# Kernel optimization log

Hardware: AMD Instinct MI355X
Metric: run time of the kernel (lower is better)

Reference implementation:

```python
import jax, jax.numpy as jnp
import numpy as np

B, N = 128, 64
HID, MLP, DS, DV = 128, 128, 32, 32
DH = MLP - DS - DV  # 64
FILL = -10.0


def _embed_mask(x, W, b, fill):
    # Linear+ReLU on non-NaN rows; fill NaN rows with `fill` (matches embed_with_masking).
    nan = jnp.isnan(x).any(-1)
    e = jax.nn.relu(jnp.where(jnp.isnan(x), 0.0, x) @ W + b)
    return jnp.where(nan[..., None], jnp.asarray(fill, x.dtype), e)


def setup_inputs() -> dict:
    key = jax.random.key(0)
    ks = jax.random.split(key, 12)
    s = 0.05
    return {
        "hidden_states": jax.random.normal(ks[0], (B, N, HID), jnp.float32),
        "obs1": jax.random.normal(ks[1], (B, N, 2), jnp.float32),
        "obs2": jax.random.normal(ks[2], (B, N, 2), jnp.float32),
        "w_sp": jax.random.normal(ks[3], (2, DS), jnp.float32) * s,
        "b_sp": jnp.zeros((DS,), jnp.float32),
        "w_vel": jax.random.normal(ks[4], (2, DV), jnp.float32) * s,
        "b_vel": jnp.zeros((DV,), jnp.float32),
        "w_hid": jax.random.normal(ks[5], (HID, DH), jnp.float32) * s,
        "b_hid": jnp.zeros((DH,), jnp.float32),
        "wq": jax.random.normal(ks[6], (MLP, MLP), jnp.float32) * s,
        "wk": jax.random.normal(ks[7], (MLP, MLP), jnp.float32) * s,
        "wv": jax.random.normal(ks[8], (MLP, MLP), jnp.float32) * s,
        "in_proj_w": jax.random.normal(ks[9], (MLP, 3 * MLP), jnp.float32) * s,
        "in_proj_b": jnp.zeros((3 * MLP,), jnp.float32),
        "mha_out_w": jax.random.normal(ks[10], (MLP, MLP), jnp.float32) * s,
        "mha_out_b": jnp.zeros((MLP,), jnp.float32),
        "out_w": jax.random.normal(ks[11], (MLP, MLP), jnp.float32) * s,
        "out_b": jnp.zeros((MLP,), jnp.float32),
    }


def reference(hidden_states, obs1, obs2, w_sp, b_sp, w_vel, b_vel, w_hid, b_hid,
              wq, wk, wv, in_proj_w, in_proj_b, mha_out_w, mha_out_b, out_w, out_b):
    b, n = obs2.shape[0], obs2.shape[1]
    # relative positions: rel[b,i,j] = obs2[b,j] - obs2[b,i]
    rel = obs2[:, None, :, :] - obs2[:, :, None, :]              # [B,N,N,2]
    sp = _embed_mask(rel, w_sp, b_sp, FILL)                      # [B,N,N,DS]
    hid = _embed_mask(hidden_states, w_hid, b_hid, 0.0)          # [B,N,DH]
    hid_unf = jnp.broadcast_to(hid[:, None, :, :], (b, n, n, DH))
    vel = obs2 - obs1
    relvel = vel[:, None, :, :] - vel[:, :, None, :]             # [B,N,N,2]
    dv = _embed_mask(relvel * 4, w_vel, b_vel, FILL)             # [B,N,N,DV]
    emb = jnp.concatenate([sp, hid_unf, dv], axis=-1)            # [B,N,N,MLP]

    # MHA (1 head) in-proj weights split (stored as [in,out])
    w_iq, w_ik, w_iv = in_proj_w[:, :MLP], in_proj_w[:, MLP:2 * MLP], in_proj_w[:, 2 * MLP:]
    b_iq, b_ik, b_iv = in_proj_b[:MLP], in_proj_b[MLP:2 * MLP], in_proj_b[2 * MLP:]

    # Only the diagonal query position is kept by the final eye-mask gather,
    # and softmax rows are independent, so compute q only at j == i.
    idx = jnp.arange(n)
    emb_diag = emb[:, idx, idx]                                  # [B,N,MLP]
    q = (emb_diag @ wq) @ w_iq + b_iq                            # [B,N,MLP]
    k = (emb @ wk) @ w_ik + b_ik                                 # [B,N,N,MLP]
    v = (emb @ wv) @ w_iv + b_iv                                 # [B,N,N,MLP]

    scores = jnp.einsum('bid,bijd->bij', q, k) / jnp.sqrt(jnp.asarray(MLP, q.dtype))
    attn = jax.nn.softmax(scores, axis=-1)                       # [B,N,N]
    ctx = jnp.einsum('bij,bijd->bid', attn, v)                   # [B,N,MLP]
    mha_out = ctx @ mha_out_w + mha_out_b
    out = mha_out @ out_w + out_b                                # [B,N,out_dim]
    return out.reshape(b * n, -1)
```

## Files before the change

kernel.cpp:

```cpp
#include <hip/hip_runtime.h>
#include <string.h>

typedef float v2f __attribute__((ext_vector_type(2)));
#define PKFMA(a,b,c) __builtin_elementwise_fma((a),(b),(c))
#define PKMAX(a,b)   __builtin_elementwise_max((a),(b))
static __device__ __forceinline__ v2f vsplat(float s) { return (v2f){s, s}; }
static __device__ __forceinline__ v2f shfl_xor_v2(v2f x, int m) {
    double d = __builtin_bit_cast(double, x);
    d = __shfl_xor(d, m, 64);
    return __builtin_bit_cast(v2f, d);
}

#define WS_WQC   0
#define WS_WKC   16384
#define WS_WVC   32768
#define WS_MOW   49152
#define WS_GQ    65536
#define WS_G0Q   73728
#define WS_FALL  73856
#define WS_FB    90240
#define WS_HID   90368
#define WS_NEED_HID_BYTES ((size_t)(90368 + 128*64*64) * 4)

__global__ __launch_bounds__(256) void precompute1(
    const float* __restrict__ wq, const float* __restrict__ wk,
    const float* __restrict__ wv, const float* __restrict__ in_proj_w,
    const float* __restrict__ mha_out_w, const float* __restrict__ out_w,
    const float* __restrict__ hs, const float* __restrict__ w_hid,
    const float* __restrict__ b_hid, float* __restrict__ ws)
{
    __shared__ __align__(16) float sbuf[4224];
    const int tid = threadIdx.x;

    if (blockIdx.x < 256) {
        const int mat  = blockIdx.x >> 6;
        const int rp   = blockIdx.x & 63;
        const int rsel = tid >> 7;
        const int col  = tid & 127;
        const int r    = 2 * rp + rsel;
        const float* A; const float* Bm; int ldb; float* C;
        if (mat == 0)      { A = wq;        Bm = in_proj_w;       ldb = 384; C = ws + WS_WQC; }
        else if (mat == 1) { A = wk;        Bm = in_proj_w + 128; ldb = 384; C = ws + WS_WKC; }
        else if (mat == 2) { A = wv;        Bm = in_proj_w + 256; ldb = 384; C = ws + WS_WVC; }
        else               { A = mha_out_w; Bm = out_w;           ldb = 128; C = ws + WS_MOW; }
        sbuf[tid] = A[r * 128 + col];
        __syncthreads();
        float acc = 0.f;
        #pragma unroll 8
        for (int d = 0; d < 128; ++d) acc = fmaf(sbuf[rsel * 128 + d], Bm[d * ldb + col], acc);
        C[r * 128 + col] = acc;
    } else {
        const int b2 = blockIdx.x - 256;
        const int b = b2 >> 1, half = b2 & 1;
        const float4* src = (const float4*)(hs + b * 8192 + half * 4096);
        for (int k = tid; k < 1024; k += 256) {
            const int row = k >> 5, c = k & 31;
            *(float4*)&sbuf[row * 132 + 4 * c] = src[k];
        }
        __syncthreads();
        const int ty = tid >> 4, tx = tid & 15;
        float a0c[4] = {0,0,0,0}, a1c[4] = {0,0,0,0};
        for (int d0 = 0; d0 < 128; d0 += 4) {
            const float4 a0 = *(const float4*)&sbuf[(2*ty+0)*132 + d0];
            const float4 a1 = *(const float4*)&sbuf[(2*ty+1)*132 + d0];
            const float* a0p = (const float*)&a0;
            const float* a1p = (const float*)&a1;
            #pragma unroll
            for (int dd = 0; dd < 4; ++dd) {
                const float4 w4 = *(const float4*)&w_hid[(d0+dd)*64 + 4*tx];
                a0c[0] = fmaf(a0p[dd], w4.x, a0c[0]); a0c[1] = fmaf(a0p[dd], w4.y, a0c[1]);
                a0c[2] = fmaf(a0p[dd], w4.z, a0c[2]); a0c[3] = fmaf(a0p[dd], w4.w, a0c[3]);
                a1c[0] = fmaf(a1p[dd], w4.x, a1c[0]); a1c[1] = fmaf(a1p[dd], w4.y, a1c[1]);
                a1c[2] = fmaf(a1p[dd], w4.z, a1c[2]); a1c[3] = fmaf(a1p[dd], w4.w, a1c[3]);
            }
        }
        const float4 bh = *(const float4*)&b_hid[4*tx];
        float* dst = ws + WS_HID + b * 4096 + (32*half + 2*ty) * 64 + 4*tx;
        *(float4*)dst        = make_float4(fmaxf(a0c[0]+bh.x,0.f), fmaxf(a0c[1]+bh.y,0.f),
                                           fmaxf(a0c[2]+bh.z,0.f), fmaxf(a0c[3]+bh.w,0.f));
        *(float4*)(dst + 64) = make_float4(fmaxf(a1c[0]+bh.x,0.f), fmaxf(a1c[1]+bh.y,0.f),
                                           fmaxf(a1c[2]+bh.z,0.f), fmaxf(a1c[3]+bh.w,0.f));
    }
}

__global__ __launch_bounds__(128) void precompute2(
    const float* __restrict__ b_sp, const float* __restrict__ b_vel,
    const float* __restrict__ in_proj_b, const float* __restrict__ mha_out_b,
    const float* __restrict__ out_w, const float* __restrict__ out_b,
    float* __restrict__ ws)
{
    const float* Wqc = ws + WS_WQC;
    const float* Wkc = ws + WS_WKC;
    const float* Wvc = ws + WS_WVC;
    const float* Mow = ws + WS_MOW;
    const int bid = blockIdx.x, tid = threadIdx.x;
    __shared__ float sa[128];

    if (bid < 64) {
        const int k = bid;
        sa[tid] = Wqc[(32 + k) * 128 + tid];
        __syncthreads();
        const int j = tid;
        const int pj = (j < 64) ? 32 + j : ((j < 96) ? j - 64 : j);
        const float* brow = Wkc + pj * 128;
        float acc = 0.f;
        #pragma unroll 8
        for (int d = 0; d < 128; ++d) acc = fmaf(sa[d], brow[d], acc);
        ws[WS_GQ + k * 128 + j] = acc;
    } else if (bid < 192) {
        const int k2 = bid - 64;
        const int srcRow = (k2 < 32) ? k2 : ((k2 < 64) ? 96 + (k2 - 32) : 32 + (k2 - 64));
        sa[tid] = Wvc[srcRow * 128 + tid];
        __syncthreads();
        float acc = 0.f;
        #pragma unroll 8
        for (int m = 0; m < 128; ++m) acc = fmaf(sa[m], Mow[m * 128 + tid], acc);
        ws[WS_FALL + k2 * 128 + tid] = acc;
    } else if (bid == 192) {
        float acc = out_b[tid];
        #pragma unroll 8
        for (int m = 0; m < 128; ++m) {
            acc = fmaf(in_proj_b[256 + m], Mow[m * 128 + tid], acc);
            acc = fmaf(mha_out_b[m], out_w[m * 128 + tid], acc);
        }
        ws[WS_FB + tid] = acc;
    } else {
        float qc = in_proj_b[tid];
        #pragma unroll 4
        for (int s = 0; s < 32; ++s) {
            qc = fmaf(fmaxf(b_sp[s], 0.f),  Wqc[s * 128 + tid], qc);
            qc = fmaf(fmaxf(b_vel[s], 0.f), Wqc[(96 + s) * 128 + tid], qc);
        }
        sa[tid] = qc;
        __syncthreads();
        const int j = tid;
        const int pj = (j < 64) ? 32 + j : ((j < 96) ? j - 64 : j);
        const float* brow = Wkc + pj * 128;
        float acc = 0.f;
        #pragma unroll 8
        for (int d = 0; d < 128; ++d) acc = fmaf(sa[d], brow[d], acc);
        ws[WS_G0Q + j] = acc;
    }
}

#define L_OBS  4224
#define L_WV   4480

template <bool HIDWS>
__global__ __launch_bounds__(256) void attn_main(
    const float* __restrict__ hs, const float* __restrict__ obs1,
    const float* __restrict__ obs2,
    const float* __restrict__ w_sp, const float* __restrict__ b_sp,
    const float* __restrict__ w_vel, const float* __restrict__ b_vel,
    const float* __restrict__ w_hid, const float* __restrict__ b_hid,
    const float* __restrict__ ws, float* __restrict__ out)
{
    const int tid = threadIdx.x;
    const int l   = tid & 63;
    const int w   = tid >> 6;
    const int b   = blockIdx.x >> 2;
    const int i0  = (blockIdx.x & 3) * 16;
    const int rg0 = i0 + 4 * w;

    const float* GQ   = ws + WS_GQ;
    const float* g0q  = ws + WS_G0Q;
    const float* Fall = ws + WS_FALL;
    const float* fbv  = ws + WS_FB;

    __shared__ __align__(16) float smem[7552];
    float* const s_hid = smem;
    float* const s_obs = smem + L_OBS;
    float* const tt = smem + L_WV + w * 768;
    float* const qq = smem + L_WV + w * 768 + 256;
    float* const aa = smem + L_WV + w * 768 + 512;

    if (tid < 64) {
        const int g = b * 64 + tid;
        const float2 o2 = ((const float2*)obs2)[g];
        const float2 o1 = ((const float2*)obs1)[g];
        *(float4*)&s_obs[tid * 4] = make_float4(o2.x, o2.y, o2.x - o1.x, o2.y - o1.y);
    }
    if (HIDWS) {
        const float4* src = (const float4*)(ws + WS_HID + b * 4096);
        #pragma unroll
        for (int k = tid; k < 1024; k += 256) {
            const int row = k >> 4, c4 = (k & 15) * 4;
            const float4 v = src[k];
            *(v2f*)&s_hid[row * 66 + c4]     = (v2f){v.x, v.y};
            *(v2f*)&s_hid[row * 66 + c4 + 2] = (v2f){v.z, v.w};
        }
    } else {
        const int r = tid >> 2, qseg = (tid & 3) * 16;
        float acc[16];
        #pragma unroll
        for (int c = 0; c < 16; ++c) acc[c] = b_hid[qseg + c];
        for (int k = 0; k < 128; ++k) {
            const float a = hs[b * 8192 + r * 128 + k];
            #pragma unroll
            for (int c4 = 0; c4 < 4; ++c4) {
                const float4 w4 = *(const float4*)&w_hid[k * 64 + qseg + 4 * c4];
                acc[4*c4+0] = fmaf(a, w4.x, acc[4*c4+0]);
                acc[4*c4+1] = fmaf(a, w4.y, acc[4*c4+1]);
                acc[4*c4+2] = fmaf(a, w4.z, acc[4*c4+2]);
                acc[4*c4+3] = fmaf(a, w4.w, acc[4*c4+3]);
            }
        }
        #pragma unroll
        for (int c = 0; c < 16; c += 2)
            *(v2f*)&s_hid[r * 66 + qseg + c] =
                (v2f){fmaxf(acc[c], 0.f), fmaxf(acc[c+1], 0.f)};
    }
    __syncthreads();

    {
        const v2f bias = *(const v2f*)&g0q[2 * l];
        v2f acc0 = bias, acc1 = bias, acc2 = bias, acc3 = bias;
        for (int k0 = 0; k0 < 64; k0 += 2) {
            const v2f g0 = *(const v2f*)&GQ[k0 * 128 + 2 * l];
            const v2f g1 = *(const v2f*)&GQ[(k0 + 1) * 128 + 2 * l];
            const v2f h0 = *(const v2f*)&s_hid[(rg0 + 0) * 66 + k0];
            const v2f h1 = *(const v2f*)&s_hid[(rg0 + 1) * 66 + k0];
            const v2f h2 = *(const v2f*)&s_hid[(rg0 + 2) * 66 + k0];
            const v2f h3 = *(const v2f*)&s_hid[(rg0 + 3) * 66 + k0];
            acc0 = PKFMA(vsplat(h0.x), g0, PKFMA(vsplat(h0.y), g1, acc0));
            acc1 = PKFMA(vsplat(h1.x), g0, PKFMA(vsplat(h1.y), g1, acc1));
            acc2 = PKFMA(vsplat(h2.x), g0, PKFMA(vsplat(h2.y), g1, acc2));
            acc3 = PKFMA(vsplat(h3.x), g0, PKFMA(vsplat(h3.y), g1, acc3));
        }
        if (l < 32) {
            const int c = 2 * l;
            *(v2f*)&tt[0 * 64 + c] = acc0;  *(v2f*)&tt[1 * 64 + c] = acc1;
            *(v2f*)&tt[2 * 64 + c] = acc2;  *(v2f*)&tt[3 * 64 + c] = acc3;
        } else {
            const int c = 2 * l - 64;
            *(v2f*)&qq[0 * 64 + c] = acc0;  *(v2f*)&qq[1 * 64 + c] = acc1;
            *(v2f*)&qq[2 * 64 + c] = acc2;  *(v2f*)&qq[3 * 64 + c] = acc3;
        }
    }

    float sc[4];
    {
        v2f s0 = (v2f){0.f,0.f}, s1 = s0, s2 = s0, s3 = s0;
        const float* hl = &s_hid[l * 66];
        for (int c0 = 0; c0 < 64; c0 += 2) {
            const v2f h2 = *(const v2f*)&hl[c0];
            s0 = PKFMA(*(const v2f*)&tt[0 * 64 + c0], h2, s0);
            s1 = PKFMA(*(const v2f*)&tt[1 * 64 + c0], h2, s1);
            s2 = PKFMA(*(const v2f*)&tt[2 * 64 + c0], h2, s2);
            s3 = PKFMA(*(const v2f*)&tt[3 * 64 + c0], h2, s3);
        }
        sc[0] = s0.x + s0.y; sc[1] = s1.x + s1.y;
        sc[2] = s2.x + s2.y; sc[3] = s3.x + s3.y;
    }

    {
        const float4 oj = *(const float4*)&s_obs[4 * l];
        float rx[4], ry[4], dx[4], dy[4];
        #pragma unroll
        for (int r = 0; r < 4; ++r) {
            const float4 oi = *(const float4*)&s_obs[4 * (rg0 + r)];
            rx[r] = oj.x - oi.x;  ry[r] = oj.y - oi.y;
            dx[r] = (oj.z - oi.z) * 4.f;  dy[r] = (oj.w - oi.w) * 4.f;
        }
        v2f acc[4] = {{0,0},{0,0},{0,0},{0,0}};
        for (int s0 = 0; s0 < 32; s0 += 2) {
            const v2f w0p = *(const v2f*)&w_sp[s0];
            const v2f w1p = *(const v2f*)&w_sp[32 + s0];
            const v2f bsp = *(const v2f*)&b_sp[s0];
            const v2f u0p = *(const v2f*)&w_vel[s0];
            const v2f u1p = *(const v2f*)&w_vel[32 + s0];
            const v2f bvp = *(const v2f*)&b_vel[s0];
            #pragma unroll
            for (int r = 0; r < 4; ++r) {
                const v2f qs2 = *(const v2f*)&qq[r * 64 + s0];
                const v2f qd2 = *(const v2f*)&qq[r * 64 + 32 + s0];
                const v2f esp = PKMAX(PKFMA(vsplat(rx[r]), w0p,
                                     PKFMA(vsplat(ry[r]), w1p, bsp)), vsplat(0.f));
                acc[r] = PKFMA(qs2, esp, acc[r]);
                const v2f edv = PKMAX(PKFMA(vsplat(dx[r]), u0p,
                                     PKFMA(vsplat(dy[r]), u1p, bvp)), vsplat(0.f));
                acc[r] = PKFMA(qd2, edv, acc[r]);
            }
        }
        const float scale = 0.08838834764831845f;
        v2f p01 = (v2f){(sc[0] + acc[0].x + acc[0].y) * scale,
                        (sc[1] + acc[1].x + acc[1].y) * scale};
        v2f p23 = (v2f){(sc[2] + acc[2].x + acc[2].y) * scale,
                        (sc[3] + acc[3].x + acc[3].y) * scale};
        v2f m01 = p01, m23 = p23;
        #pragma unroll
        for (int off = 32; off > 0; off >>= 1) {
            m01 = PKMAX(m01, shfl_xor_v2(m01, off));
            m23 = PKMAX(m23, shfl_xor_v2(m23, off));
        }
        v2f e01 = (v2f){__expf(p01.x - m01.x), __expf(p01.y - m01.y)};
        v2f e23 = (v2f){__expf(p23.x - m23.x), __expf(p23.y - m23.y)};
        v2f u01 = e01, u23 = e23;
        #pragma unroll
        for (int off = 32; off > 0; off >>= 1) {
            u01 = u01 + shfl_xor_v2(u01, off);
            u23 = u23 + shfl_xor_v2(u23, off);
        }
        *(float4*)&aa[4 * l] = make_float4(e01.x / u01.x, e01.y / u01.y,
                                           e23.x / u23.x, e23.y / u23.y);
    }

    {
        const int r = l >> 4, s = l & 15;
        const v2f w0p = (v2f){w_sp[s],        w_sp[s + 16]};
        const v2f w1p = (v2f){w_sp[32 + s],   w_sp[48 + s]};
        const v2f bsp = (v2f){b_sp[s],        b_sp[s + 16]};
        const v2f u0p = (v2f){w_vel[s],       w_vel[s + 16]};
        const v2f u1p = (v2f){w_vel[32 + s],  w_vel[48 + s]};
        const v2f bvp = (v2f){b_vel[s],       b_vel[s + 16]};
        const float4 oi = *(const float4*)&s_obs[4 * (rg0 + r)];
        v2f asp = (v2f){0.f, 0.f}, adv = asp;
        for (int j = 0; j < 64; ++j) {
            const float a = aa[4 * j + r];
            const float4 o4 = *(const float4*)&s_obs[4 * j];
            const float rxx = o4.x - oi.x, ryy = o4.y - oi.y;
            const float dxx = (o4.z - oi.z) * 4.f, dyy = (o4.w - oi.w) * 4.f;
            const v2f esp = PKMAX(PKFMA(vsplat(rxx), w0p,
                                 PKFMA(vsplat(ryy), w1p, bsp)), vsplat(0.f));
            asp = PKFMA(vsplat(a), esp, asp);
            const v2f edv = PKMAX(PKFMA(vsplat(dxx), u0p,
                                 PKFMA(vsplat(dyy), u1p, bvp)), vsplat(0.f));
            adv = PKFMA(vsplat(a), edv, adv);
        }
        tt[r * 64 + s]           = asp.x;
        tt[r * 64 + s + 16]      = asp.y;
        tt[r * 64 + 32 + s]      = adv.x;
        tt[r * 64 + 48 + s]      = adv.y;
    }

    {
        float ah0 = 0.f, ah1 = 0.f, ah2 = 0.f, ah3 = 0.f;
        for (int j = 0; j < 64; j += 2) {
            const float4 a0 = *(const float4*)&aa[4 * j];
            const float4 a1 = *(const float4*)&aa[4 * j + 4];
            const float h0 = s_hid[j * 66 + l];
            const float h1 = s_hid[(j + 1) * 66 + l];
            ah0 = fmaf(a0.x, h0, fmaf(a1.x, h1, ah0));
            ah1 = fmaf(a0.y, h0, fmaf(a1.y, h1, ah1));
            ah2 = fmaf(a0.z, h0, fmaf(a1.z, h1, ah2));
            ah3 = fmaf(a0.w, h0, fmaf(a1.w, h1, ah3));
        }
        qq[0 * 64 + l] = ah0;  qq[1 * 64 + l] = ah1;
        qq[2 * 64 + l] = ah2;  qq[3 * 64 + l] = ah3;
    }

    {
        const v2f fb2 = *(const v2f*)&fbv[2 * l];
        v2f o0 = fb2, o1 = fb2, o2 = fb2, o3 = fb2;
        for (int k = 0; k < 64; k += 2) {
            const v2f f0 = *(const v2f*)&Fall[k * 128 + 2 * l];
            const v2f f1 = *(const v2f*)&Fall[(k + 1) * 128 + 2 * l];
            const v2f A0 = *(const v2f*)&tt[0 * 64 + k];
            const v2f A1 = *(const v2f*)&tt[1 * 64 + k];
            const v2f A2 = *(const v2f*)&tt[2 * 64 + k];
            const v2f A3 = *(const v2f*)&tt[3 * 64 + k];
            o0 = PKFMA(vsplat(A0.x), f0, PKFMA(vsplat(A0.y), f1, o0));
            o1 = PKFMA(vsplat(A1.x), f0, PKFMA(vsplat(A1.y), f1, o1));
            o2 = PKFMA(vsplat(A2.x), f0, PKFMA(vsplat(A2.y), f1, o2));
            o3 = PKFMA(vsplat(A3.x), f0, PKFMA(vsplat(A3.y), f1, o3));
        }
        for (int k = 0; k < 64; k += 2) {
            const v2f f0 = *(const v2f*)&Fall[(64 + k) * 128 + 2 * l];
            const v2f f1 = *(const v2f*)&Fall[(65 + k) * 128 + 2 * l];
            const v2f A0 = *(const v2f*)&qq[0 * 64 + k];
            const v2f A1 = *(const v2f*)&qq[1 * 64 + k];
            const v2f A2 = *(const v2f*)&qq[2 * 64 + k];
            const v2f A3 = *(const v2f*)&qq[3 * 64 + k];
            o0 = PKFMA(vsplat(A0.x), f0, PKFMA(vsplat(A0.y), f1, o0));
            o1 = PKFMA(vsplat(A1.x), f0, PKFMA(vsplat(A1.y), f1, o1));
            o2 = PKFMA(vsplat(A2.x), f0, PKFMA(vsplat(A2.y), f1, o2));
            o3 = PKFMA(vsplat(A3.x), f0, PKFMA(vsplat(A3.y), f1, o3));
        }
        const int gr = (b * 64 + rg0) * 128 + 2 * l;
        *(v2f*)&out[gr]           = o0;
        *(v2f*)&out[gr + 128]     = o1;
        *(v2f*)&out[gr + 256]     = o2;
        *(v2f*)&out[gr + 384]     = o3;
    }
}

extern "C" void kernel_launch(void* const* d_in, const int* in_sizes, int n_in,
                              void* d_out, int out_size, void* d_ws, size_t ws_size,
                              hipStream_t stream) {
    const float* hs        = (const float*)d_in[0];
    const float* obs1      = (const float*)d_in[1];
    const float* obs2      = (const float*)d_in[2];
    const float* w_sp      = (const float*)d_in[3];
    const float* b_sp      = (const float*)d_in[4];
    const float* w_vel     = (const float*)d_in[5];
    const float* b_vel     = (const float*)d_in[6];
    const float* w_hid     = (const float*)d_in[7];
    const float* b_hid     = (const float*)d_in[8];
    const float* wq        = (const float*)d_in[9];
    const float* wk        = (const float*)d_in[10];
    const float* wv        = (const float*)d_in[11];
    const float* in_proj_w = (const float*)d_in[12];
    const float* in_proj_b = (const float*)d_in[13];
    const float* mha_out_w = (const float*)d_in[14];
    const float* mha_out_b = (const float*)d_in[15];
    const float* out_w     = (const float*)d_in[16];
    const float* out_b     = (const float*)d_in[17];
    float* ws  = (float*)d_ws;
    float* out = (float*)d_out;

    const bool hidws = (ws_size >= WS_NEED_HID_BYTES);

    precompute1<<<hidws ? 512 : 256, 256, 0, stream>>>(
        wq, wk, wv, in_proj_w, mha_out_w, out_w, hs, w_hid, b_hid, ws);
    precompute2<<<194, 128, 0, stream>>>(
        b_sp, b_vel, in_proj_b, mha_out_b, out_w, out_b, ws);
    if (hidws) {
        attn_main<true><<<512, 256, 0, stream>>>(hs, obs1, obs2, w_sp, b_sp, w_vel, b_vel,
                                                 w_hid, b_hid, ws, out);
    } else {
        attn_main<false><<<512, 256, 0, stream>>>(hs, obs1, obs2, w_sp, b_sp, w_vel, b_vel,
                                                  w_hid, b_hid, ws, out);
    }
}
```

Baseline: 128.9 us.

## Fuse three kernels into one cooperative launch with grid-wide syncs

Merges the two precompute kernels and the attention kernel into a single cooperative kernel of 512 blocks, using grid.sync() between the weight-folding phases and the main attention phase. This removes two kernel launch boundaries and their idle gaps. It requires all 512 blocks to be co-resident; otherwise the cooperative launch fails and the code falls back to the old three-kernel path. Grid-wide barriers also cost something, and blocks sit idle in the lightly loaded middle phase.

```diff
diff --git a/kernel.cpp b/kernel.cpp
--- a/kernel.cpp
+++ b/kernel.cpp
@@ -1,10 +1,13 @@
 #include <hip/hip_runtime.h>
-#include <string.h>
+#include <hip/hip_cooperative_groups.h>
+
+namespace cg = cooperative_groups;
 
 typedef float v2f __attribute__((ext_vector_type(2)));
 #define PKFMA(a,b,c) __builtin_elementwise_fma((a),(b),(c))
 #define PKMAX(a,b)   __builtin_elementwise_max((a),(b))
 static __device__ __forceinline__ v2f vsplat(float s) { return (v2f){s, s}; }
+static __device__ __forceinline__ v2f vmk(float a, float b) { return (v2f){a, b}; }
 static __device__ __forceinline__ v2f shfl_xor_v2(v2f x, int m) {
     double d = __builtin_bit_cast(double, x);
     d = __shfl_xor(d, m, 64);
@@ -21,6 +24,347 @@
 #define WS_FB    90240
 #define WS_HID   90368
 #define WS_NEED_HID_BYTES ((size_t)(90368 + 128*64*64) * 4)
+
+__global__ __launch_bounds__(256) void fused_all(
+    const float* __restrict__ hs, const float* __restrict__ obs1,
+    const float* __restrict__ obs2,
+    const float* __restrict__ w_sp, const float* __restrict__ b_sp,
+    const float* __restrict__ w_vel, const float* __restrict__ b_vel,
+    const float* __restrict__ w_hid, const float* __restrict__ b_hid,
+    const float* __restrict__ wq, const float* __restrict__ wk,
+    const float* __restrict__ wv, const float* __restrict__ in_proj_w,
+    const float* __restrict__ in_proj_b, const float* __restrict__ mha_out_w,
+    const float* __restrict__ mha_out_b, const float* __restrict__ out_w,
+    const float* __restrict__ out_b,
+    float* __restrict__ ws, float* __restrict__ out)
+{
+    const int tid = threadIdx.x;
+    const int bid = blockIdx.x;
+    __shared__ __align__(16) float smem[7552];
+
+    if (bid < 256) {
+        const int mat  = bid >> 6;
+        const int rp   = bid & 63;
+        const int tsel = tid >> 7;
+        const int col  = tid & 127;
+        const int r    = 2 * rp + tsel;
+        const float* A; const float* Bm; int ldb; float* C;
+        if (mat == 0)      { A = wq;        Bm = in_proj_w;       ldb = 384; C = ws + WS_WQC; }
+        else if (mat == 1) { A = wk;        Bm = in_proj_w + 128; ldb = 384; C = ws + WS_WKC; }
+        else if (mat == 2) { A = wv;        Bm = in_proj_w + 256; ldb = 384; C = ws + WS_WVC; }
+        else               { A = mha_out_w; Bm = out_w;           ldb = 128; C = ws + WS_MOW; }
+        smem[tid] = A[r * 128 + col];
+        __syncthreads();
+        const float* sp = &smem[tsel * 128];
+        v2f acc = {0.f, 0.f};
+        #pragma unroll 8
+        for (int d = 0; d < 128; d += 2)
+            acc = PKFMA(*(const v2f*)&sp[d], vmk(Bm[d * ldb + col], Bm[(d + 1) * ldb + col]), acc);
+        C[r * 128 + col] = acc.x + acc.y;
+    } else {
+        const int b2 = bid - 256;
+        const int b = b2 >> 1, half = b2 & 1;
+        const float4* src = (const float4*)(hs + b * 8192 + half * 4096);
+        for (int k = tid; k < 1024; k += 256) {
+            const int row = k >> 5, c = k & 31;
+            *(float4*)&smem[row * 132 + 4 * c] = src[k];
+        }
+        __syncthreads();
+        const int ty = tid >> 4, tx = tid & 15;
+        v2f a0ab = {0,0}, a0cd = {0,0}, a1ab = {0,0}, a1cd = {0,0};
+        for (int d0 = 0; d0 < 128; d0 += 2) {
+            const v2f a0 = *(const v2f*)&smem[(2*ty+0)*132 + d0];
+            const v2f a1 = *(const v2f*)&smem[(2*ty+1)*132 + d0];
+            const float4 w40 = *(const float4*)&w_hid[d0 * 64 + 4 * tx];
+            const float4 w41 = *(const float4*)&w_hid[(d0 + 1) * 64 + 4 * tx];
+            const v2f w0a = vmk(w40.x, w40.y), w0b = vmk(w40.z, w40.w);
+            const v2f w1a = vmk(w41.x, w41.y), w1b = vmk(w41.z, w41.w);
+            a0ab = PKFMA(vsplat(a0.x), w0a, PKFMA(vsplat(a0.y), w1a, a0ab));
+            a0cd = PKFMA(vsplat(a0.x), w0b, PKFMA(vsplat(a0.y), w1b, a0cd));
+            a1ab = PKFMA(vsplat(a1.x), w0a, PKFMA(vsplat(a1.y), w1a, a1ab));
+            a1cd = PKFMA(vsplat(a1.x), w0b, PKFMA(vsplat(a1.y), w1b, a1cd));
+        }
+        const float4 bh = *(const float4*)&b_hid[4 * tx];
+        float* dst = ws + WS_HID + b * 4096 + (32 * half + 2 * ty) * 64 + 4 * tx;
+        *(float4*)dst = make_float4(fmaxf(a0ab.x + bh.x, 0.f), fmaxf(a0ab.y + bh.y, 0.f),
+                                    fmaxf(a0cd.x + bh.z, 0.f), fmaxf(a0cd.y + bh.w, 0.f));
+        *(float4*)(dst + 64) = make_float4(fmaxf(a1ab.x + bh.x, 0.f), fmaxf(a1ab.y + bh.y, 0.f),
+                                           fmaxf(a1cd.x + bh.z, 0.f), fmaxf(a1cd.y + bh.w, 0.f));
+    }
+    __threadfence();
+    cg::this_grid().sync();
+
+    {
+        const float* Wqc = ws + WS_WQC;
+        const float* Wkc = ws + WS_WKC;
+        const float* Wvc = ws + WS_WVC;
+        const float* Mow = ws + WS_MOW;
+        const int tsel = tid >> 7, col = tid & 127;
+        if (bid < 32) {
+            const int k = 2 * bid + tsel;
+            smem[tid] = Wqc[(32 + k) * 128 + col];
+            __syncthreads();
+            const int pj = (col < 64) ? 32 + col : ((col < 96) ? col - 64 : col);
+            const float* brow = Wkc + pj * 128;
+            const float* sp = &smem[tsel * 128];
+            v2f acc = {0.f, 0.f};
+            #pragma unroll 8
+            for (int d = 0; d < 128; d += 2)
+                acc = PKFMA(*(const v2f*)&sp[d], *(const v2f*)&brow[d], acc);
+            ws[WS_GQ + k * 128 + col] = acc.x + acc.y;
+        } else if (bid < 96) {
+            const int k2 = 2 * (bid - 32) + tsel;
+            const int srcRow = (k2 < 32) ? k2 : ((k2 < 64) ? 96 + (k2 - 32) : 32 + (k2 - 64));
+            smem[tid] = Wvc[srcRow * 128 + col];
+            __syncthreads();
+            const float* sp = &smem[tsel * 128];
+            v2f acc = {0.f, 0.f};
+            #pragma unroll 8
+            for (int m = 0; m < 128; m += 2)
+                acc = PKFMA(*(const v2f*)&sp[m],
+                            vmk(Mow[m * 128 + col], Mow[(m + 1) * 128 + col]), acc);
+            ws[WS_FALL + k2 * 128 + col] = acc.x + acc.y;
+        } else if (bid == 96) {
+            if (tid >= 128) {
+                float qc = in_proj_b[col];
+                #pragma unroll 4
+                for (int s = 0; s < 32; ++s) {
+                    qc = fmaf(fmaxf(b_sp[s], 0.f),  Wqc[s * 128 + col], qc);
+                    qc = fmaf(fmaxf(b_vel[s], 0.f), Wqc[(96 + s) * 128 + col], qc);
+                }
+                smem[col] = qc;
+            }
+            __syncthreads();
+            if (tid < 128) {
+                float acc = out_b[col];
+                #pragma unroll 8
+                for (int m = 0; m < 128; ++m) {
+                    acc = fmaf(in_proj_b[256 + m], Mow[m * 128 + col], acc);
+                    acc = fmaf(mha_out_b[m], out_w[m * 128 + col], acc);
+                }
+                ws[WS_FB + col] = acc;
+            } else {
+                const int pj = (col < 64) ? 32 + col : ((col < 96) ? col - 64 : col);
+                const float* brow = Wkc + pj * 128;
+                float acc = 0.f;
+                #pragma unroll 8
+                for (int d = 0; d < 128; ++d) acc = fmaf(smem[d], brow[d], acc);
+                ws[WS_G0Q + col] = acc;
+            }
+        }
+    }
+    __threadfence();
+    cg::this_grid().sync();
+
+    {
+        const int l   = tid & 63;
+        const int w   = tid >> 6;
+        const int b   = bid >> 2;
+        const int i0  = (bid & 3) * 16;
+        const int rg0 = i0 + 4 * w;
+
+        const float* GQ   = ws + WS_GQ;
+        const float* g0q  = ws + WS_G0Q;
+        const float* Fall = ws + WS_FALL;
+        const float* fbv  = ws + WS_FB;
+
+        float* const s_hid = smem;
+        float* const s_obs = smem + 4224;
+        float* const tt = smem + 4480 + w * 768;
+        float* const qq = smem + 4480 + w * 768 + 256;
+        float* const aa = smem + 4480 + w * 768 + 512;
+
+        __syncthreads();
+        if (tid < 64) {
+            const int g = b * 64 + tid;
+            const float2 o2 = ((const float2*)obs2)[g];
+            const float2 o1 = ((const float2*)obs1)[g];
+            *(float4*)&s_obs[tid * 4] = make_float4(o2.x, o2.y, o2.x - o1.x, o2.y - o1.y);
+        }
+        {
+            const float4* src = (const float4*)(ws + WS_HID + b * 4096);
+            #pragma unroll
+            for (int k = tid; k < 1024; k += 256) {
+                const int row = k >> 4, c4 = (k & 15) * 4;
+                const float4 v = src[k];
+                *(v2f*)&s_hid[row * 66 + c4]     = vmk(v.x, v.y);
+                *(v2f*)&s_hid[row * 66 + c4 + 2] = vmk(v.z, v.w);
+            }
+        }
+        __syncthreads();
+
+        {
+            const v2f bias = *(const v2f*)&g0q[2 * l];
+            v2f acc0 = bias, acc1 = bias, acc2 = bias, acc3 = bias;
+            for (int k0 = 0; k0 < 64; k0 += 2) {
+                const v2f g0 = *(const v2f*)&GQ[k0 * 128 + 2 * l];
+                const v2f g1 = *(const v2f*)&GQ[(k0 + 1) * 128 + 2 * l];
+                const v2f h0 = *(const v2f*)&s_hid[(rg0 + 0) * 66 + k0];
+                const v2f h1 = *(const v2f*)&s_hid[(rg0 + 1) * 66 + k0];
+                const v2f h2 = *(const v2f*)&s_hid[(rg0 + 2) * 66 + k0];
+                const v2f h3 = *(const v2f*)&s_hid[(rg0 + 3) * 66 + k0];
+                acc0 = PKFMA(vsplat(h0.x), g0, PKFMA(vsplat(h0.y), g1, acc0));
+                acc1 = PKFMA(vsplat(h1.x), g0, PKFMA(vsplat(h1.y), g1, acc1));
+                acc2 = PKFMA(vsplat(h2.x), g0, PKFMA(vsplat(h2.y), g1, acc2));
+                acc3 = PKFMA(vsplat(h3.x), g0, PKFMA(vsplat(h3.y), g1, acc3));
+            }
+            if (l < 32) {
+                const int c = 2 * l;
+                *(v2f*)&tt[0 * 64 + c] = acc0;  *(v2f*)&tt[1 * 64 + c] = acc1;
+                *(v2f*)&tt[2 * 64 + c] = acc2;  *(v2f*)&tt[3 * 64 + c] = acc3;
+            } else {
+                const int c = 2 * l - 64;
+                *(v2f*)&qq[0 * 64 + c] = acc0;  *(v2f*)&qq[1 * 64 + c] = acc1;
+                *(v2f*)&qq[2 * 64 + c] = acc2;  *(v2f*)&qq[3 * 64 + c] = acc3;
+            }
+        }
+
+        float sc[4];
+        {
+            v2f s0 = (v2f){0.f,0.f}, s1 = s0, s2 = s0, s3 = s0;
+            const float* hl = &s_hid[l * 66];
+            for (int c0 = 0; c0 < 64; c0 += 2) {
+                const v2f h2 = *(const v2f*)&hl[c0];
+                s0 = PKFMA(*(const v2f*)&tt[0 * 64 + c0], h2, s0);
+                s1 = PKFMA(*(const v2f*)&tt[1 * 64 + c0], h2, s1);
+                s2 = PKFMA(*(const v2f*)&tt[2 * 64 + c0], h2, s2);
+                s3 = PKFMA(*(const v2f*)&tt[3 * 64 + c0], h2, s3);
+            }
+            sc[0] = s0.x + s0.y; sc[1] = s1.x + s1.y;
+            sc[2] = s2.x + s2.y; sc[3] = s3.x + s3.y;
+        }
+
+        {
+            const float4 oj = *(const float4*)&s_obs[4 * l];
+            float rx[4], ry[4], dx[4], dy[4];
+            #pragma unroll
+            for (int r = 0; r < 4; ++r) {
+                const float4 oi = *(const float4*)&s_obs[4 * (rg0 + r)];
+                rx[r] = oj.x - oi.x;  ry[r] = oj.y - oi.y;
+                dx[r] = (oj.z - oi.z) * 4.f;  dy[r] = (oj.w - oi.w) * 4.f;
+            }
+            v2f acc[4] = {{0,0},{0,0},{0,0},{0,0}};
+            for (int s0 = 0; s0 < 32; s0 += 2) {
+                const v2f w0p = *(const v2f*)&w_sp[s0];
+                const v2f w1p = *(const v2f*)&w_sp[32 + s0];
+                const v2f bsp = *(const v2f*)&b_sp[s0];
+                const v2f u0p = *(const v2f*)&w_vel[s0];
+                const v2f u1p = *(const v2f*)&w_vel[32 + s0];
+                const v2f bvp = *(const v2f*)&b_vel[s0];
+                #pragma unroll
+                for (int r = 0; r < 4; ++r) {
+                    const v2f qs2 = *(const v2f*)&qq[r * 64 + s0];
+                    const v2f qd2 = *(const v2f*)&qq[r * 64 + 32 + s0];
+                    const v2f esp = PKMAX(PKFMA(vsplat(rx[r]), w0p,
+                                         PKFMA(vsplat(ry[r]), w1p, bsp)), vsplat(0.f));
+                    acc[r] = PKFMA(qs2, esp, acc[r]);
+                    const v2f edv = PKMAX(PKFMA(vsplat(dx[r]), u0p,
+                                         PKFMA(vsplat(dy[r]), u1p, bvp)), vsplat(0.f));
+                    acc[r] = PKFMA(qd2, edv, acc[r]);
+                }
+            }
+            const float scale = 0.08838834764831845f;
+            v2f p01 = vmk((sc[0] + acc[0].x + acc[0].y) * scale,
+                          (sc[1] + acc[1].x + acc[1].y) * scale);
+            v2f p23 = vmk((sc[2] + acc[2].x + acc[2].y) * scale,
+                          (sc[3] + acc[3].x + acc[3].y) * scale);
+            v2f m01 = p01, m23 = p23;
+            #pragma unroll
+            for (int off = 32; off > 0; off >>= 1) {
+                m01 = PKMAX(m01, shfl_xor_v2(m01, off));
+                m23 = PKMAX(m23, shfl_xor_v2(m23, off));
+            }
+            v2f e01 = vmk(__expf(p01.x - m01.x), __expf(p01.y - m01.y));
+            v2f e23 = vmk(__expf(p23.x - m23.x), __expf(p23.y - m23.y));
+            v2f u01 = e01, u23 = e23;
+            #pragma unroll
+            for (int off = 32; off > 0; off >>= 1) {
+                u01 = u01 + shfl_xor_v2(u01, off);
+                u23 = u23 + shfl_xor_v2(u23, off);
+            }
+            *(float4*)&aa[4 * l] = make_float4(e01.x / u01.x, e01.y / u01.y,
+                                               e23.x / u23.x, e23.y / u23.y);
+        }
+
+        {
+            const int r = l >> 4, s = l & 15;
+            const v2f w0p = vmk(w_sp[s],        w_sp[s + 16]);
+            const v2f w1p = vmk(w_sp[32 + s],   w_sp[48 + s]);
+            const v2f bsp = vmk(b_sp[s],        b_sp[s + 16]);
+            const v2f u0p = vmk(w_vel[s],       w_vel[s + 16]);
+            const v2f u1p = vmk(w_vel[32 + s],  w_vel[48 + s]);
+            const v2f bvp = vmk(b_vel[s],       b_vel[s + 16]);
+            const float4 oi = *(const float4*)&s_obs[4 * (rg0 + r)];
+            v2f asp = (v2f){0.f, 0.f}, adv = asp;
+            for (int j = 0; j < 64; ++j) {
+                const float a = aa[4 * j + r];
+                const float4 o4 = *(const float4*)&s_obs[4 * j];
+                const float rxx = o4.x - oi.x, ryy = o4.y - oi.y;
+                const float dxx = (o4.z - oi.z) * 4.f, dyy = (o4.w - oi.w) * 4.f;
+                const v2f esp = PKMAX(PKFMA(vsplat(rxx), w0p,
+                                     PKFMA(vsplat(ryy), w1p, bsp)), vsplat(0.f));
+                asp = PKFMA(vsplat(a), esp, asp);
+                const v2f edv = PKMAX(PKFMA(vsplat(dxx), u0p,
+                                     PKFMA(vsplat(dyy), u1p, bvp)), vsplat(0.f));
+                adv = PKFMA(vsplat(a), edv, adv);
+            }
+            tt[r * 64 + s]      = asp.x;
+            tt[r * 64 + s + 16] = asp.y;
+            tt[r * 64 + 32 + s] = adv.x;
+            tt[r * 64 + 48 + s] = adv.y;
+        }
+
+        {
+            float ah0 = 0.f, ah1 = 0.f, ah2 = 0.f, ah3 = 0.f;
+            for (int j = 0; j < 64; j += 2) {
+                const float4 a0 = *(const float4*)&aa[4 * j];
+                const float4 a1 = *(const float4*)&aa[4 * j + 4];
+                const float h0 = s_hid[j * 66 + l];
+                const float h1 = s_hid[(j + 1) * 66 + l];
+                ah0 = fmaf(a0.x, h0, fmaf(a1.x, h1, ah0));
+                ah1 = fmaf(a0.y, h0, fmaf(a1.y, h1, ah1));
+                ah2 = fmaf(a0.z, h0, fmaf(a1.z, h1, ah2));
+                ah3 = fmaf(a0.w, h0, fmaf(a1.w, h1, ah3));
+            }
+            qq[0 * 64 + l] = ah0;  qq[1 * 64 + l] = ah1;
+            qq[2 * 64 + l] = ah2;  qq[3 * 64 + l] = ah3;
+        }
+
+        {
+            const v2f fb2 = *(const v2f*)&fbv[2 * l];
+            v2f o0 = fb2, o1 = fb2, o2 = fb2, o3 = fb2;
+            for (int k = 0; k < 64; k += 2) {
+                const v2f f0 = *(const v2f*)&Fall[k * 128 + 2 * l];
+                const v2f f1 = *(const v2f*)&Fall[(k + 1) * 128 + 2 * l];
+                const v2f A0 = *(const v2f*)&tt[0 * 64 + k];
+                const v2f A1 = *(const v2f*)&tt[1 * 64 + k];
+                const v2f A2 = *(const v2f*)&tt[2 * 64 + k];
+                const v2f A3 = *(const v2f*)&tt[3 * 64 + k];
+                o0 = PKFMA(vsplat(A0.x), f0, PKFMA(vsplat(A0.y), f1, o0));
+                o1 = PKFMA(vsplat(A1.x), f0, PKFMA(vsplat(A1.y), f1, o1));
+                o2 = PKFMA(vsplat(A2.x), f0, PKFMA(vsplat(A2.y), f1, o2));
+                o3 = PKFMA(vsplat(A3.x), f0, PKFMA(vsplat(A3.y), f1, o3));
+            }
+            for (int k = 0; k < 64; k += 2) {
+                const v2f f0 = *(const v2f*)&Fall[(64 + k) * 128 + 2 * l];
+                const v2f f1 = *(const v2f*)&Fall[(65 + k) * 128 + 2 * l];
+                const v2f A0 = *(const v2f*)&qq[0 * 64 + k];
+                const v2f A1 = *(const v2f*)&qq[1 * 64 + k];
+                const v2f A2 = *(const v2f*)&qq[2 * 64 + k];
+                const v2f A3 = *(const v2f*)&qq[3 * 64 + k];
+                o0 = PKFMA(vsplat(A0.x), f0, PKFMA(vsplat(A0.y), f1, o0));
+                o1 = PKFMA(vsplat(A1.x), f0, PKFMA(vsplat(A1.y), f1, o1));
+                o2 = PKFMA(vsplat(A2.x), f0, PKFMA(vsplat(A2.y), f1, o2));
+                o3 = PKFMA(vsplat(A3.x), f0, PKFMA(vsplat(A3.y), f1, o3));
+            }
+            const int gr = (b * 64 + rg0) * 128 + 2 * l;
+            *(v2f*)&out[gr]       = o0;
+            *(v2f*)&out[gr + 128] = o1;
+            *(v2f*)&out[gr + 256] = o2;
+            *(v2f*)&out[gr + 384] = o3;
+        }
+    }
+}
 
 __global__ __launch_bounds__(256) void precompute1(
     const float* __restrict__ wq, const float* __restrict__ wk,
@@ -142,9 +486,6 @@
         ws[WS_G0Q + j] = acc;
     }
 }
-
-#define L_OBS  4224
-#define L_WV   4480
 
 template <bool HIDWS>
 __global__ __launch_bounds__(256) void attn_main(
@@ -169,10 +510,10 @@
 
     __shared__ __align__(16) float smem[7552];
     float* const s_hid = smem;
-    float* const s_obs = smem + L_OBS;
-    float* const tt = smem + L_WV + w * 768;
-    float* const qq = smem + L_WV + w * 768 + 256;
-    float* const aa = smem + L_WV + w * 768 + 512;
+    float* const s_obs = smem + 4224;
+    float* const tt = smem + 4480 + w * 768;
+    float* const qq = smem + 4480 + w * 768 + 256;
+    float* const aa = smem + 4480 + w * 768 + 512;
 
     if (tid < 64) {
         const int g = b * 64 + tid;
@@ -186,8 +527,8 @@
         for (int k = tid; k < 1024; k += 256) {
             const int row = k >> 4, c4 = (k & 15) * 4;
             const float4 v = src[k];
-            *(v2f*)&s_hid[row * 66 + c4]     = (v2f){v.x, v.y};
-            *(v2f*)&s_hid[row * 66 + c4 + 2] = (v2f){v.z, v.w};
+            *(v2f*)&s_hid[row * 66 + c4]     = vmk(v.x, v.y);
+            *(v2f*)&s_hid[row * 66 + c4 + 2] = vmk(v.z, v.w);
         }
     } else {
         const int r = tid >> 2, qseg = (tid & 3) * 16;
@@ -208,7 +549,7 @@
         #pragma unroll
         for (int c = 0; c < 16; c += 2)
             *(v2f*)&s_hid[r * 66 + qseg + c] =
-                (v2f){fmaxf(acc[c], 0.f), fmaxf(acc[c+1], 0.f)};
+                vmk(fmaxf(acc[c], 0.f), fmaxf(acc[c+1], 0.f));
     }
     __syncthreads();
 
@@ -283,18 +624,18 @@
             }
         }
         const float scale = 0.08838834764831845f;
-        v2f p01 = (v2f){(sc[0] + acc[0].x + acc[0].y) * scale,
-                        (sc[1] + acc[1].x + acc[1].y) * scale};
-        v2f p23 = (v2f){(sc[2] + acc[2].x + acc[2].y) * scale,
-                        (sc[3] + acc[3].x + acc[3].y) * scale};
+        v2f p01 = vmk((sc[0] + acc[0].x + acc[0].y) * scale,
+                      (sc[1] + acc[1].x + acc[1].y) * scale);
+        v2f p23 = vmk((sc[2] + acc[2].x + acc[2].y) * scale,
+                      (sc[3] + acc[3].x + acc[3].y) * scale);
         v2f m01 = p01, m23 = p23;
         #pragma unroll
         for (int off = 32; off > 0; off >>= 1) {
             m01 = PKMAX(m01, shfl_xor_v2(m01, off));
             m23 = PKMAX(m23, shfl_xor_v2(m23, off));
         }
-        v2f e01 = (v2f){__expf(p01.x - m01.x), __expf(p01.y - m01.y)};
-        v2f e23 = (v2f){__expf(p23.x - m23.x), __expf(p23.y - m23.y)};
+        v2f e01 = vmk(__expf(p01.x - m01.x), __expf(p01.y - m01.y));
+        v2f e23 = vmk(__expf(p23.x - m23.x), __expf(p23.y - m23.y));
         v2f u01 = e01, u23 = e23;
         #pragma unroll
         for (int off = 32; off > 0; off >>= 1) {
@@ -307,12 +648,12 @@
 
     {
         const int r = l >> 4, s = l & 15;
-        const v2f w0p = (v2f){w_sp[s],        w_sp[s + 16]};
-        const v2f w1p = (v2f){w_sp[32 + s],   w_sp[48 + s]};
-        const v2f bsp = (v2f){b_sp[s],        b_sp[s + 16]};
-        const v2f u0p = (v2f){w_vel[s],       w_vel[s + 16]};
-        const v2f u1p = (v2f){w_vel[32 + s],  w_vel[48 + s]};
-        const v2f bvp = (v2f){b_vel[s],       b_vel[s + 16]};
+        const v2f w0p = vmk(w_sp[s],        w_sp[s + 16]);
+        const v2f w1p = vmk(w_sp[32 + s],   w_sp[48 + s]);
+        const v2f bsp = vmk(b_sp[s],        b_sp[s + 16]);
+        const v2f u0p = vmk(w_vel[s],       w_vel[s + 16]);
+        const v2f u1p = vmk(w_vel[32 + s],  w_vel[48 + s]);
+        const v2f bvp = vmk(b_vel[s],       b_vel[s + 16]);
         const float4 oi = *(const float4*)&s_obs[4 * (rg0 + r)];
         v2f asp = (v2f){0.f, 0.f}, adv = asp;
         for (int j = 0; j < 64; ++j) {
@@ -327,10 +668,10 @@
                                  PKFMA(vsplat(dyy), u1p, bvp)), vsplat(0.f));
             adv = PKFMA(vsplat(a), edv, adv);
         }
-        tt[r * 64 + s]           = asp.x;
-        tt[r * 64 + s + 16]      = asp.y;
-        tt[r * 64 + 32 + s]      = adv.x;
-        tt[r * 64 + 48 + s]      = adv.y;
+        tt[r * 64 + s]      = asp.x;
+        tt[r * 64 + s + 16] = asp.y;
+        tt[r * 64 + 32 + s] = adv.x;
+        tt[r * 64 + 48 + s] = adv.y;
     }
 
     {
@@ -377,10 +718,10 @@
             o3 = PKFMA(vsplat(A3.x), f0, PKFMA(vsplat(A3.y), f1, o3));
         }
         const int gr = (b * 64 + rg0) * 128 + 2 * l;
-        *(v2f*)&out[gr]           = o0;
-        *(v2f*)&out[gr + 128]     = o1;
-        *(v2f*)&out[gr + 256]     = o2;
-        *(v2f*)&out[gr + 384]     = o3;
+        *(v2f*)&out[gr]       = o0;
+        *(v2f*)&out[gr + 128] = o1;
+        *(v2f*)&out[gr + 256] = o2;
+        *(v2f*)&out[gr + 384] = o3;
     }
 }
 
@@ -410,15 +751,30 @@
 
     const bool hidws = (ws_size >= WS_NEED_HID_BYTES);
 
-    precompute1<<<hidws ? 512 : 256, 256, 0, stream>>>(
-        wq, wk, wv, in_proj_w, mha_out_w, out_w, hs, w_hid, b_hid, ws);
-    precompute2<<<194, 128, 0, stream>>>(
-        b_sp, b_vel, in_proj_b, mha_out_b, out_w, out_b, ws);
+    bool done = false;
     if (hidws) {
-        attn_main<true><<<512, 256, 0, stream>>>(hs, obs1, obs2, w_sp, b_sp, w_vel, b_vel,
-                                                 w_hid, b_hid, ws, out);
-    } else {
-        attn_main<false><<<512, 256, 0, stream>>>(hs, obs1, obs2, w_sp, b_sp, w_vel, b_vel,
-                                                  w_hid, b_hid, ws, out);
+        void* args[] = {
+            (void*)&hs, (void*)&obs1, (void*)&obs2, (void*)&w_sp, (void*)&b_sp,
+            (void*)&w_vel, (void*)&b_vel, (void*)&w_hid, (void*)&b_hid,
+            (void*)&wq, (void*)&wk, (void*)&wv, (void*)&in_proj_w, (void*)&in_proj_b,
+            (void*)&mha_out_w, (void*)&mha_out_b, (void*)&out_w, (void*)&out_b,
+            (void*)&ws, (void*)&out};
+        hipError_t err = hipLaunchCooperativeKernel((const void*)fused_all,
+                                                    dim3(512), dim3(256),
+                                                    args, 0, stream);
+        done = (err == hipSuccess);
+    }
+    if (!done) {
+        precompute1<<<hidws ? 512 : 256, 256, 0, stream>>>(
+            wq, wk, wv, in_proj_w, mha_out_w, out_w, hs, w_hid, b_hid, ws);
+        precompute2<<<194, 128, 0, stream>>>(
+            b_sp, b_vel, in_proj_b, mha_out_b, out_w, out_b, ws);
+        if (hidws) {
+            attn_main<true><<<512, 256, 0, stream>>>(hs, obs1, obs2, w_sp, b_sp, w_vel,
+                                                     b_vel, w_hid, b_hid, ws, out);
+        } else {
+            attn_main<false><<<512, 256, 0, stream>>>(hs, obs1, obs2, w_sp, b_sp, w_vel,
+                                                      b_vel, w_hid, b_hid, ws, out);
+        }
     }
 }
```

New measurement: 353.8 us. 174% more time.
